# Kernel optimization log

Measured on AMD Instinct MI355X. Metric: run time of the kernel, lower is better.

Reference implementation:

```python
import jax, jax.numpy as jnp
import numpy as np

B, S, D, F, H = 32768, 3, 512, 512, 8
DH = F // H
NEG = 1e9


def setup_inputs() -> dict:
    key = jax.random.key(0)
    ks = jax.random.split(key, 13)
    mk = lambda i, shape: jax.random.normal(ks[i], shape, dtype=jnp.float32)
    return {
        "q": mk(0, (B, S, D)),
        "k": mk(1, (B, S, D)),
        "v": mk(2, (B, S, D)),
        "mask": jax.random.randint(ks[3], (B, S), 0, 2, dtype=jnp.int32),
        "Wq": mk(4, (D, F)) * 0.02, "bq": jnp.zeros((F,), jnp.float32),
        "Wk": mk(5, (D, F)) * 0.02, "bk": jnp.zeros((F,), jnp.float32),
        "Wv": mk(6, (D, F)) * 0.02, "bv": jnp.zeros((F,), jnp.float32),
        "Wo": mk(7, (F, F)) * 0.02, "bo": jnp.zeros((F,), jnp.float32),
    }


def _split_heads(x):
    # [B, S, F] -> [B, H, S, DH]
    b, s, _ = x.shape
    return x.reshape(b, s, H, DH).transpose(0, 2, 1, 3)


def reference(q, k, v, mask, Wq, bq, Wk, bk, Wv, bv, Wo, bo):
    qh = _split_heads(q @ Wq + bq)
    kh = _split_heads(k @ Wk + bk)
    vh = _split_heads(v @ Wv + bv)
    scores = jnp.einsum("bhqd,bhkd->bhqk", qh, kh) / np.sqrt(DH).astype(np.float32)
    m = mask.astype(scores.dtype) * NEG  # [B, S]
    scores = scores - m[:, None, None, :] - m[:, None, :, None]  # col + row mask
    w = jax.nn.softmax(scores, axis=-1)
    attn = jnp.einsum("bhqk,bhkd->bhqd", w, vh)  # [B, H, S, DH]
    attn = attn.transpose(0, 2, 1, 3).reshape(attn.shape[0], S, F)
    return attn @ Wo + bo
```

## Files before the change

### kernel.cpp

```cpp
#include <hip/hip_runtime.h>


typedef __bf16 bf16x8 __attribute__((ext_vector_type(8)));
typedef float f32x4 __attribute__((ext_vector_type(4)));

union U8 { bf16x8 v; unsigned short u[8]; uint4 q; };

__device__ __forceinline__ unsigned short f2bf(float f) {
  union { float f; unsigned int u; } v; v.f = f;
  unsigned int u = v.u;
  return (unsigned short)((u + 0x7FFFu + ((u >> 16) & 1u)) >> 16);
}
__device__ __forceinline__ unsigned int cvt_pk_bf16(float lo, float hi) {
  unsigned int r;
  asm volatile("v_cvt_pk_bf16_f32 %0, %1, %2" : "=v"(r) : "v"(lo), "v"(hi));
  return r;
}

__global__ void __launch_bounds__(256) wtrans(const float* __restrict__ W0,
                                              const float* __restrict__ W1,
                                              const float* __restrict__ W2,
                                              const float* __restrict__ W3,
                                              unsigned short* __restrict__ out) {
  __shared__ float tile[64][65];
  const float* W = (blockIdx.z == 0) ? W0 : (blockIdx.z == 1) ? W1
                   : (blockIdx.z == 2) ? W2 : W3;
  unsigned short* O = out + (size_t)blockIdx.z * 512 * 512;
  int t = threadIdx.x;
  int k0 = blockIdx.x * 64, n0 = blockIdx.y * 64;
#pragma unroll
  for (int i = 0; i < 4; ++i) {
    int r = (t >> 4) + i * 16;
    int c = (t & 15) * 4;
    float4 v = *(const float4*)(W + (k0 + r) * 512 + n0 + c);
    tile[r][c] = v.x; tile[r][c + 1] = v.y; tile[r][c + 2] = v.z; tile[r][c + 3] = v.w;
  }
  __syncthreads();
  int lane = t & 63, f = t >> 6;
  int lr = lane & 15, hi = lane >> 4;
#pragma unroll
  for (int i = 0; i < 2; ++i) {
    int g = f + i * 4;
    int n16l = g & 3, ksl = g >> 2;
    U8 pk;
#pragma unroll
    for (int e = 0; e < 8; ++e)
      pk.u[e] = f2bf(tile[ksl * 32 + hi * 8 + e][n16l * 16 + lr]);
    int n16 = (n0 >> 4) + n16l;
    int ksg = (k0 >> 5) + ksl;
    *(uint4*)(O + (((n16 * 16 + ksg) * 64 + lane) * 8)) = pk.q;
  }
}

#define SH_SCR  49152
#define SH_PS   65536
#define SH_MSK  71680
#define SH_BIAS 71872

__device__ __forceinline__ void stage48(const float* __restrict__ src, int row0,
                                        int t, char* smem) {
#pragma unroll 1
  for (int c = 0; c < 3; ++c) {
    float4 vals[4];
#pragma unroll
    for (int j = 0; j < 4; ++j) {
      int idx = t + (c * 4 + j) * 512;
      int row = idx >> 7, c4 = idx & 127;
      vals[j] = *(const float4*)(src + (size_t)(row0 + row) * 512 + c4 * 4);
    }
#pragma unroll
    for (int j = 0; j < 4; ++j) {
      int idx = t + (c * 4 + j) * 512;
      int row = idx >> 7, c4 = idx & 127;
      uint2 pk;
      pk.x = cvt_pk_bf16(vals[j].x, vals[j].y);
      pk.y = cvt_pk_bf16(vals[j].z, vals[j].w);
      *(uint2*)(smem + ((row * 1024 + c4 * 8) ^ ((row & 7) << 4))) = pk;
    }
  }
}

__device__ __forceinline__ void gemm_proj(const char* smem,
                                          const unsigned short* __restrict__ Bt,
                                          int w, int l, int lr, int lk8,
                                          f32x4 acc[3][4]) {
#pragma unroll 2
  for (int ks = 0; ks < 16; ++ks) {
    int kb = ks * 32 + lk8;
    bf16x8 a[3];
#pragma unroll
    for (int mt = 0; mt < 3; ++mt) {
      int row = mt * 16 + lr;
      a[mt] = *(const bf16x8*)(smem + ((row * 1024 + kb * 2) ^ ((row & 7) << 4)));
    }
#pragma unroll
    for (int np = 0; np < 2; ++np) {
      bf16x8 b[2];
#pragma unroll
      for (int j = 0; j < 2; ++j)
        b[j] = *(const bf16x8*)(Bt + (((w * 4 + np * 2 + j) * 16 + ks) * 64 + l) * 8);
#pragma unroll
      for (int j = 0; j < 2; ++j)
#pragma unroll
        for (int mt = 0; mt < 3; ++mt)
          acc[mt][np * 2 + j] =
              __builtin_amdgcn_mfma_f32_16x16x32_bf16(a[mt], b[j], acc[mt][np * 2 + j], 0, 0, 0);
    }
  }
}

__device__ __forceinline__ void tile_to_afrags(char* scr, const float* biasT, int bofs,
                                               const f32x4 acc[4], float scale,
                                               int lr, int hi, bf16x8* out) {
#pragma unroll
  for (int nt = 0; nt < 4; ++nt) {
    float bv = biasT[bofs + nt * 16];
#pragma unroll
    for (int r = 0; r < 4; ++r) {
      int row = 4 * hi + r;
      int col = nt * 16 + lr;
      int addr = (row * 128 + col * 2) ^ ((row & 7) << 4);
      *(unsigned short*)(scr + addr) = f2bf((acc[nt][r] + bv) * scale);
    }
  }
  asm volatile("s_waitcnt lgkmcnt(0)" ::: "memory");
#pragma unroll
  for (int kb = 0; kb < 2; ++kb) {
    int addr = (lr * 128 + (kb * 32 + hi * 8) * 2) ^ ((lr & 7) << 4);
    out[kb] = *(const bf16x8*)(scr + addr);
  }
  asm volatile("s_waitcnt lgkmcnt(0)" ::: "memory");
}

__global__ void __launch_bounds__(512, 4) fused_attn(
    const float* __restrict__ q, const float* __restrict__ kin, const float* __restrict__ vin,
    const int* __restrict__ mask, const unsigned short* __restrict__ wt,
    const float* __restrict__ bq, const float* __restrict__ bk,
    const float* __restrict__ bv, const float* __restrict__ bo,
    float* __restrict__ out) {
  __shared__ alignas(16) char smem[80064];
  const int t = threadIdx.x;
  const int w = t >> 6;
  const int l = t & 63;
  const int lr = l & 15;
  const int hi = l >> 4;
  const int lk8 = hi * 8;
  const int row0 = blockIdx.x * 48;
  const int batch0 = blockIdx.x * 16;
  char* scr = smem + SH_SCR + w * 2048;
  float* pscr = (float*)(smem + SH_PS + w * 768);
  int* maskb = (int*)(smem + SH_MSK);
  float* biasT = (float*)(smem + SH_BIAS);
  const int bidx = w * 64 + lr;

  if (t < 48) maskb[t] = mask[batch0 * 3 + t];
  biasT[0 * 512 + t] = bq[t];
  biasT[1 * 512 + t] = bk[t];
  biasT[2 * 512 + t] = bv[t];
  biasT[3 * 512 + t] = bo[t];

  const unsigned short* Wtq = wt;
  const unsigned short* Wtk = wt + 512 * 512;
  const unsigned short* Wtv = wt + 2 * 512 * 512;
  const unsigned short* Wto = wt + 3 * 512 * 512;

  stage48(q, row0, t, smem);
  __syncthreads();
  bf16x8 qa[3][2];
  {
    f32x4 aq[3][4] = {};
    gemm_proj(smem, Wtq, w, l, lr, lk8, aq);
#pragma unroll
    for (int mt = 0; mt < 3; ++mt)
      tile_to_afrags(scr, biasT, 0 * 512 + bidx, aq[mt], 0.125f, lr, hi, qa[mt]);
  }
  __syncthreads();

  stage48(kin, row0, t, smem);
  __syncthreads();
  {
    f32x4 ack[3][4] = {};
    gemm_proj(smem, Wtk, w, l, lr, lk8, ack);

    bf16x8 kf[3][2];
#pragma unroll
    for (int km = 0; km < 3; ++km)
      tile_to_afrags(scr, biasT, 1 * 512 + bidx, ack[km], 1.0f, lr, hi, kf[km]);

#pragma unroll
    for (int km = 0; km < 3; ++km) {
      f32x4 s[3] = {};
#pragma unroll
      for (int qm = 0; qm < 3; ++qm) {
        s[qm] = __builtin_amdgcn_mfma_f32_16x16x32_bf16(qa[qm][0], kf[km][0], s[qm], 0, 0, 0);
        s[qm] = __builtin_amdgcn_mfma_f32_16x16x32_bf16(qa[qm][1], kf[km][1], s[qm], 0, 0, 0);
      }
#pragma unroll
      for (int qm = 0; qm < 3; ++qm)
#pragma unroll
        for (int r = 0; r < 4; ++r) {
          int qrow = qm * 16 + hi * 4 + r;
          int krow = km * 16 + lr;
          int qb = qrow / 3, kb2 = krow / 3;
          if (qb == kb2) pscr[qrow * 4 + (krow - kb2 * 3)] = s[qm][r];
        }
    }
    asm volatile("s_waitcnt lgkmcnt(0)" ::: "memory");
#pragma unroll
    for (int mt = 0; mt < 3; ++mt) {
      int row = mt * 16 + lr;
      int b = row / 3;
      int qi = row - b * 3;
      float s0 = pscr[row * 4 + 0], s1 = pscr[row * 4 + 1], s2 = pscr[row * 4 + 2];
      float m0 = (float)maskb[b * 3 + 0] * 1e9f;
      float m1 = (float)maskb[b * 3 + 1] * 1e9f;
      float m2 = (float)maskb[b * 3 + 2] * 1e9f;
      float mq = (qi == 0) ? m0 : (qi == 1) ? m1 : m2;
      float t0 = (s0 - m0) - mq;
      float t1 = (s1 - m1) - mq;
      float t2 = (s2 - m2) - mq;
      float mx = fmaxf(fmaxf(t0, t1), t2);
      float e0 = __expf(t0 - mx), e1 = __expf(t1 - mx), e2 = __expf(t2 - mx);
      float inv = 1.0f / (e0 + e1 + e2);
      asm volatile("s_waitcnt lgkmcnt(0)" ::: "memory");
      pscr[row * 4 + 0] = e0 * inv;
      pscr[row * 4 + 1] = e1 * inv;
      pscr[row * 4 + 2] = e2 * inv;
    }
  }
  __syncthreads();

  stage48(vin, row0, t, smem);
  __syncthreads();
  f32x4 acv[3][4] = {};
  gemm_proj(smem, Wtv, w, l, lr, lk8, acv);

  bf16x8 vb2[2][4];
  {
    U8 zz;
#pragma unroll
    for (int e = 0; e < 8; ++e) zz.u[e] = 0;
#pragma unroll
    for (int nt = 0; nt < 4; ++nt) vb2[1][nt] = zz.v;
  }
#pragma unroll
  for (int mt = 0; mt < 3; ++mt) {
#pragma unroll
    for (int nt = 0; nt < 4; ++nt) {
      float bvl = biasT[2 * 512 + bidx + nt * 16];
      int d = nt * 16 + lr;
      uint2 pk;
      pk.x = cvt_pk_bf16(acv[mt][nt][0] + bvl, acv[mt][nt][1] + bvl);
      pk.y = cvt_pk_bf16(acv[mt][nt][2] + bvl, acv[mt][nt][3] + bvl);
      *(uint2*)(scr + ((d * 32 + hi * 8) ^ ((d & 1) << 4))) = pk;
    }
    asm volatile("s_waitcnt lgkmcnt(0)" ::: "memory");
#pragma unroll
    for (int nt = 0; nt < 4; ++nt) {
      int d = nt * 16 + lr;
      bf16x8 tmp = *(const bf16x8*)(scr + ((d * 32 + (hi & 1) * 16) ^ ((d & 1) << 4)));
      if (mt == 0)      { if (hi < 2)  vb2[0][nt] = tmp; }
      else if (mt == 1) { if (hi >= 2) vb2[0][nt] = tmp; }
      else              { if (hi < 2)  vb2[1][nt] = tmp; }
    }
    asm volatile("s_waitcnt lgkmcnt(0)" ::: "memory");
  }
  bf16x8 pa[3][2];
#pragma unroll
  for (int mt = 0; mt < 3; ++mt) {
    int row = mt * 16 + lr;
    int b3 = (row / 3) * 3;
    float pr0 = pscr[row * 4 + 0];
    float pr1 = pscr[row * 4 + 1];
    float pr2 = pscr[row * 4 + 2];
#pragma unroll
    for (int kb = 0; kb < 2; ++kb) {
      U8 f;
#pragma unroll
      for (int e = 0; e < 8; ++e) {
        int k = kb * 32 + lk8 + e;
        int j = k - b3;
        float pv_ = (j == 0) ? pr0 : (j == 1) ? pr1 : (j == 2) ? pr2 : 0.f;
        f.u[e] = f2bf(pv_);
      }
      pa[mt][kb] = f.v;
    }
  }
  f32x4 pv[3][4] = {};
#pragma unroll
  for (int kb = 0; kb < 2; ++kb)
#pragma unroll
    for (int nt = 0; nt < 4; ++nt)
#pragma unroll
      for (int mt = 0; mt < 3; ++mt)
        pv[mt][nt] = __builtin_amdgcn_mfma_f32_16x16x32_bf16(pa[mt][kb], vb2[kb][nt], pv[mt][nt], 0, 0, 0);

  __syncthreads();
#pragma unroll
  for (int mt = 0; mt < 3; ++mt)
#pragma unroll
    for (int nt = 0; nt < 4; ++nt)
#pragma unroll
      for (int r = 0; r < 4; ++r) {
        int row = mt * 16 + hi * 4 + r;
        int col = w * 64 + nt * 16 + lr;
        *(unsigned short*)(smem + ((row * 1024 + col * 2) ^ ((row & 7) << 4))) =
            f2bf(pv[mt][nt][r]);
      }
  __syncthreads();

  f32x4 ao[3][4] = {};
  gemm_proj(smem, Wto, w, l, lr, lk8, ao);
#pragma unroll
  for (int mt = 0; mt < 3; ++mt)
#pragma unroll
    for (int nt = 0; nt < 4; ++nt) {
      float bvo = biasT[3 * 512 + bidx + nt * 16];
#pragma unroll
      for (int r = 0; r < 4; ++r) {
        int grow = row0 + mt * 16 + hi * 4 + r;
        int col = w * 64 + nt * 16 + lr;
        out[(size_t)grow * 512 + col] = ao[mt][nt][r] + bvo;
      }
    }
}

extern "C" void kernel_launch(void* const* d_in, const int* in_sizes, int n_in,
                              void* d_out, int out_size, void* d_ws, size_t ws_size,
                              hipStream_t stream) {
  const float* q = (const float*)d_in[0];
  const float* k = (const float*)d_in[1];
  const float* v = (const float*)d_in[2];
  const int* mask = (const int*)d_in[3];
  const float* Wq = (const float*)d_in[4];
  const float* bq = (const float*)d_in[5];
  const float* Wk = (const float*)d_in[6];
  const float* bk = (const float*)d_in[7];
  const float* Wv = (const float*)d_in[8];
  const float* bv = (const float*)d_in[9];
  const float* Wo = (const float*)d_in[10];
  const float* bo = (const float*)d_in[11];
  float* out = (float*)d_out;
  unsigned short* wt = (unsigned short*)d_ws;

  wtrans<<<dim3(8, 8, 4), 256, 0, stream>>>(Wq, Wk, Wv, Wo, wt);
  fused_attn<<<2048, 512, 0, stream>>>(q, k, v, mask, wt, bq, bk, bv, bo, out);
}
```

Measured before the change: 421.0 us.

## Double-buffer input staging in K-halves to overlap global loads with MFMA

Splits each 48x512 input staging into two 256-column halves held in two LDS buffers, and issues the global loads for the next half (or the next tensor) into registers before running the GEMM on the current half. The goal is to hide global-memory latency for the q/k/v reads behind the projection MFMAs instead of stalling on full staging between phases. The block syncs are replaced by a custom barrier using sched_barrier and an lgkmcnt wait. The 24 prefetched float4 values per thread add register pressure, which could affect the 4-blocks-per-CU occupancy target.

Result: slower. 591.2 us (+40.4%).

```diff
diff --git a/kernel.cpp b/kernel.cpp
--- a/kernel.cpp
+++ b/kernel.cpp
@@ -15,6 +15,13 @@
   unsigned int r;
   asm volatile("v_cvt_pk_bf16_f32 %0, %1, %2" : "=v"(r) : "v"(lo), "v"(hi));
   return r;
+}
+
+__device__ __forceinline__ void block_sync() {
+  __builtin_amdgcn_sched_barrier(0);
+  asm volatile("s_waitcnt lgkmcnt(0)" ::: "memory");
+  __builtin_amdgcn_s_barrier();
+  __builtin_amdgcn_sched_barrier(0);
 }
 
 __global__ void __launch_bounds__(256) wtrans(const float* __restrict__ W0,
@@ -52,53 +59,54 @@
   }
 }
 
+#define SH_A    0
+#define SH_B    24576
 #define SH_SCR  49152
 #define SH_PS   65536
 #define SH_MSK  71680
 #define SH_BIAS 71872
 
-__device__ __forceinline__ void stage48(const float* __restrict__ src, int row0,
-                                        int t, char* smem) {
-#pragma unroll 1
-  for (int c = 0; c < 3; ++c) {
-    float4 vals[4];
-#pragma unroll
-    for (int j = 0; j < 4; ++j) {
-      int idx = t + (c * 4 + j) * 512;
-      int row = idx >> 7, c4 = idx & 127;
-      vals[j] = *(const float4*)(src + (size_t)(row0 + row) * 512 + c4 * 4);
-    }
-#pragma unroll
-    for (int j = 0; j < 4; ++j) {
-      int idx = t + (c * 4 + j) * 512;
-      int row = idx >> 7, c4 = idx & 127;
-      uint2 pk;
-      pk.x = cvt_pk_bf16(vals[j].x, vals[j].y);
-      pk.y = cvt_pk_bf16(vals[j].z, vals[j].w);
-      *(uint2*)(smem + ((row * 1024 + c4 * 8) ^ ((row & 7) << 4))) = pk;
-    }
-  }
-}
-
-__device__ __forceinline__ void gemm_proj(const char* smem,
+__device__ __forceinline__ void stage_issue(const float* __restrict__ src, int row0,
+                                            int half, int t, float4* pre) {
+#pragma unroll
+  for (int i = 0; i < 6; ++i) {
+    int idx = t + i * 512;
+    int row = idx >> 6, c4 = idx & 63;
+    pre[i] = *(const float4*)(src + (size_t)(row0 + row) * 512 + half * 256 + c4 * 4);
+  }
+  __builtin_amdgcn_sched_barrier(0);
+}
+__device__ __forceinline__ void stage_write(char* buf, int t, const float4* pre) {
+#pragma unroll
+  for (int i = 0; i < 6; ++i) {
+    int idx = t + i * 512;
+    int row = idx >> 6, c4 = idx & 63;
+    uint2 pk;
+    pk.x = cvt_pk_bf16(pre[i].x, pre[i].y);
+    pk.y = cvt_pk_bf16(pre[i].z, pre[i].w);
+    *(uint2*)(buf + ((row * 512 + c4 * 8) ^ ((row & 7) << 4))) = pk;
+  }
+}
+
+__device__ __forceinline__ void gemm_half(const char* buf,
                                           const unsigned short* __restrict__ Bt,
-                                          int w, int l, int lr, int lk8,
+                                          int gksb, int w, int l, int lr, int lk8,
                                           f32x4 acc[3][4]) {
 #pragma unroll 2
-  for (int ks = 0; ks < 16; ++ks) {
-    int kb = ks * 32 + lk8;
+  for (int ks = 0; ks < 8; ++ks) {
+    int kl = ks * 32 + lk8;
     bf16x8 a[3];
 #pragma unroll
     for (int mt = 0; mt < 3; ++mt) {
       int row = mt * 16 + lr;
-      a[mt] = *(const bf16x8*)(smem + ((row * 1024 + kb * 2) ^ ((row & 7) << 4)));
+      a[mt] = *(const bf16x8*)(buf + ((row * 512 + kl * 2) ^ ((row & 7) << 4)));
     }
 #pragma unroll
     for (int np = 0; np < 2; ++np) {
       bf16x8 b[2];
 #pragma unroll
       for (int j = 0; j < 2; ++j)
-        b[j] = *(const bf16x8*)(Bt + (((w * 4 + np * 2 + j) * 16 + ks) * 64 + l) * 8);
+        b[j] = *(const bf16x8*)(Bt + (((w * 4 + np * 2 + j) * 16 + (gksb + ks)) * 64 + l) * 8);
 #pragma unroll
       for (int j = 0; j < 2; ++j)
 #pragma unroll
@@ -147,6 +155,8 @@
   const int lk8 = hi * 8;
   const int row0 = blockIdx.x * 48;
   const int batch0 = blockIdx.x * 16;
+  char* bufA = smem + SH_A;
+  char* bufB = smem + SH_B;
   char* scr = smem + SH_SCR + w * 2048;
   float* pscr = (float*)(smem + SH_PS + w * 768);
   int* maskb = (int*)(smem + SH_MSK);
@@ -164,29 +174,44 @@
   const unsigned short* Wtv = wt + 2 * 512 * 512;
   const unsigned short* Wto = wt + 3 * 512 * 512;
 
-  stage48(q, row0, t, smem);
-  __syncthreads();
+  float4 pre[6];
+
+  stage_issue(q, row0, 0, t, pre);
+  stage_write(bufA, t, pre);
+  block_sync();
+  stage_issue(q, row0, 1, t, pre);
+
   bf16x8 qa[3][2];
   {
     f32x4 aq[3][4] = {};
-    gemm_proj(smem, Wtq, w, l, lr, lk8, aq);
+    gemm_half(bufA, Wtq, 0, w, l, lr, lk8, aq);
+    stage_write(bufB, t, pre);
+    block_sync();
+    stage_issue(kin, row0, 0, t, pre);
+    gemm_half(bufB, Wtq, 8, w, l, lr, lk8, aq);
+    stage_write(bufA, t, pre);
+    block_sync();
+    stage_issue(kin, row0, 1, t, pre);
 #pragma unroll
     for (int mt = 0; mt < 3; ++mt)
       tile_to_afrags(scr, biasT, 0 * 512 + bidx, aq[mt], 0.125f, lr, hi, qa[mt]);
   }
-  __syncthreads();
-
-  stage48(kin, row0, t, smem);
-  __syncthreads();
+
   {
     f32x4 ack[3][4] = {};
-    gemm_proj(smem, Wtk, w, l, lr, lk8, ack);
+    gemm_half(bufA, Wtk, 0, w, l, lr, lk8, ack);
+    stage_write(bufB, t, pre);
+    block_sync();
+    stage_issue(vin, row0, 0, t, pre);
+    gemm_half(bufB, Wtk, 8, w, l, lr, lk8, ack);
+    stage_write(bufA, t, pre);
+    block_sync();
+    stage_issue(vin, row0, 1, t, pre);
 
     bf16x8 kf[3][2];
 #pragma unroll
     for (int km = 0; km < 3; ++km)
       tile_to_afrags(scr, biasT, 1 * 512 + bidx, ack[km], 1.0f, lr, hi, kf[km]);
-
 #pragma unroll
     for (int km = 0; km < 3; ++km) {
       f32x4 s[3] = {};
@@ -228,12 +253,12 @@
       pscr[row * 4 + 2] = e2 * inv;
     }
   }
-  __syncthreads();
-
-  stage48(vin, row0, t, smem);
-  __syncthreads();
+
   f32x4 acv[3][4] = {};
-  gemm_proj(smem, Wtv, w, l, lr, lk8, acv);
+  gemm_half(bufA, Wtv, 0, w, l, lr, lk8, acv);
+  stage_write(bufB, t, pre);
+  block_sync();
+  gemm_half(bufB, Wtv, 8, w, l, lr, lk8, acv);
 
   bf16x8 vb2[2][4];
   {
@@ -295,22 +320,27 @@
       for (int mt = 0; mt < 3; ++mt)
         pv[mt][nt] = __builtin_amdgcn_mfma_f32_16x16x32_bf16(pa[mt][kb], vb2[kb][nt], pv[mt][nt], 0, 0, 0);
 
-  __syncthreads();
-#pragma unroll
-  for (int mt = 0; mt < 3; ++mt)
-#pragma unroll
-    for (int nt = 0; nt < 4; ++nt)
-#pragma unroll
-      for (int r = 0; r < 4; ++r) {
-        int row = mt * 16 + hi * 4 + r;
-        int col = w * 64 + nt * 16 + lr;
-        *(unsigned short*)(smem + ((row * 1024 + col * 2) ^ ((row & 7) << 4))) =
-            f2bf(pv[mt][nt][r]);
-      }
-  __syncthreads();
+  block_sync();
+  {
+    char* abuf = (w < 4) ? bufA : bufB;
+    int cw = (w & 3) * 64;
+#pragma unroll
+    for (int mt = 0; mt < 3; ++mt)
+#pragma unroll
+      for (int nt = 0; nt < 4; ++nt)
+#pragma unroll
+        for (int r = 0; r < 4; ++r) {
+          int row = mt * 16 + hi * 4 + r;
+          int colh = cw + nt * 16 + lr;
+          *(unsigned short*)(abuf + ((row * 512 + colh * 2) ^ ((row & 7) << 4))) =
+              f2bf(pv[mt][nt][r]);
+        }
+  }
+  block_sync();
 
   f32x4 ao[3][4] = {};
-  gemm_proj(smem, Wto, w, l, lr, lk8, ao);
+  gemm_half(bufA, Wto, 0, w, l, lr, lk8, ao);
+  gemm_half(bufB, Wto, 8, w, l, lr, lk8, ao);
 #pragma unroll
   for (int mt = 0; mt < 3; ++mt)
 #pragma unroll
```

## Load Q/K/V projection A-fragments directly from global instead of staging in LDS

Applied to the files above, without the earlier changes.

The Q, K and V projection GEMMs now read each wave's A-operand fragments straight from global fp32 memory and convert them to bf16 in registers. This drops the cooperative LDS staging pass and several block-wide barriers. The cost is that each of the 8 waves redundantly fetches the same 48x512 input rows, relying on L1/L2 to absorb the repeats, and global-load latency now sits inside the MFMA loop. The B-fragment loads are also regrouped so all four are issued before the MFMAs.

Measured after the change: 786.3 us. +86.8%, slower.

```diff
diff --git a/kernel.cpp b/kernel.cpp
--- a/kernel.cpp
+++ b/kernel.cpp
@@ -4,7 +4,7 @@
 typedef __bf16 bf16x8 __attribute__((ext_vector_type(8)));
 typedef float f32x4 __attribute__((ext_vector_type(4)));
 
-union U8 { bf16x8 v; unsigned short u[8]; uint4 q; };
+union U8 { bf16x8 v; unsigned short u[8]; unsigned int w[4]; uint4 q; };
 
 __device__ __forceinline__ unsigned short f2bf(float f) {
   union { float f; unsigned int u; } v; v.f = f;
@@ -52,38 +52,47 @@
   }
 }
 
+#define SH_ATT  0
 #define SH_SCR  49152
 #define SH_PS   65536
 #define SH_MSK  71680
 #define SH_BIAS 71872
 
-__device__ __forceinline__ void stage48(const float* __restrict__ src, int row0,
-                                        int t, char* smem) {
-#pragma unroll 1
-  for (int c = 0; c < 3; ++c) {
-    float4 vals[4];
-#pragma unroll
-    for (int j = 0; j < 4; ++j) {
-      int idx = t + (c * 4 + j) * 512;
-      int row = idx >> 7, c4 = idx & 127;
-      vals[j] = *(const float4*)(src + (size_t)(row0 + row) * 512 + c4 * 4);
-    }
-#pragma unroll
-    for (int j = 0; j < 4; ++j) {
-      int idx = t + (c * 4 + j) * 512;
-      int row = idx >> 7, c4 = idx & 127;
-      uint2 pk;
-      pk.x = cvt_pk_bf16(vals[j].x, vals[j].y);
-      pk.y = cvt_pk_bf16(vals[j].z, vals[j].w);
-      *(uint2*)(smem + ((row * 1024 + c4 * 8) ^ ((row & 7) << 4))) = pk;
-    }
-  }
-}
-
-__device__ __forceinline__ void gemm_proj(const char* smem,
-                                          const unsigned short* __restrict__ Bt,
-                                          int w, int l, int lr, int lk8,
-                                          f32x4 acc[3][4]) {
+__device__ __forceinline__ void gemm_dir(const float* __restrict__ Aw,
+                                         const unsigned short* __restrict__ Bt,
+                                         int w, int l, f32x4 acc[3][4]) {
+#pragma unroll 2
+  for (int ks = 0; ks < 16; ++ks) {
+    bf16x8 a[3];
+#pragma unroll
+    for (int mt = 0; mt < 3; ++mt) {
+      const float* p = Aw + mt * (16 * 512) + ks * 32;
+      float4 lo = *(const float4*)(p);
+      float4 hp = *(const float4*)(p + 4);
+      U8 f;
+      f.w[0] = cvt_pk_bf16(lo.x, lo.y);
+      f.w[1] = cvt_pk_bf16(lo.z, lo.w);
+      f.w[2] = cvt_pk_bf16(hp.x, hp.y);
+      f.w[3] = cvt_pk_bf16(hp.z, hp.w);
+      a[mt] = f.v;
+    }
+    bf16x8 b[4];
+#pragma unroll
+    for (int nt = 0; nt < 4; ++nt)
+      b[nt] = *(const bf16x8*)(Bt + (((w * 4 + nt) * 16 + ks) * 64 + l) * 8);
+#pragma unroll
+    for (int nt = 0; nt < 4; ++nt)
+#pragma unroll
+      for (int mt = 0; mt < 3; ++mt)
+        acc[mt][nt] =
+            __builtin_amdgcn_mfma_f32_16x16x32_bf16(a[mt], b[nt], acc[mt][nt], 0, 0, 0);
+  }
+}
+
+__device__ __forceinline__ void gemm_lds(const char* buf,
+                                         const unsigned short* __restrict__ Bt,
+                                         int w, int l, int lr, int lk8,
+                                         f32x4 acc[3][4]) {
 #pragma unroll 2
   for (int ks = 0; ks < 16; ++ks) {
     int kb = ks * 32 + lk8;
@@ -91,21 +100,18 @@
 #pragma unroll
     for (int mt = 0; mt < 3; ++mt) {
       int row = mt * 16 + lr;
-      a[mt] = *(const bf16x8*)(smem + ((row * 1024 + kb * 2) ^ ((row & 7) << 4)));
-    }
-#pragma unroll
-    for (int np = 0; np < 2; ++np) {
-      bf16x8 b[2];
-#pragma unroll
-      for (int j = 0; j < 2; ++j)
-        b[j] = *(const bf16x8*)(Bt + (((w * 4 + np * 2 + j) * 16 + ks) * 64 + l) * 8);
-#pragma unroll
-      for (int j = 0; j < 2; ++j)
-#pragma unroll
-        for (int mt = 0; mt < 3; ++mt)
-          acc[mt][np * 2 + j] =
-              __builtin_amdgcn_mfma_f32_16x16x32_bf16(a[mt], b[j], acc[mt][np * 2 + j], 0, 0, 0);
-    }
+      a[mt] = *(const bf16x8*)(buf + ((row * 1024 + kb * 2) ^ ((row & 7) << 4)));
+    }
+    bf16x8 b[4];
+#pragma unroll
+    for (int nt = 0; nt < 4; ++nt)
+      b[nt] = *(const bf16x8*)(Bt + (((w * 4 + nt) * 16 + ks) * 64 + l) * 8);
+#pragma unroll
+    for (int nt = 0; nt < 4; ++nt)
+#pragma unroll
+      for (int mt = 0; mt < 3; ++mt)
+        acc[mt][nt] =
+            __builtin_amdgcn_mfma_f32_16x16x32_bf16(a[mt], b[nt], acc[mt][nt], 0, 0, 0);
   }
 }
 
@@ -147,6 +153,7 @@
   const int lk8 = hi * 8;
   const int row0 = blockIdx.x * 48;
   const int batch0 = blockIdx.x * 16;
+  char* attnb = smem + SH_ATT;
   char* scr = smem + SH_SCR + w * 2048;
   float* pscr = (float*)(smem + SH_PS + w * 768);
   int* maskb = (int*)(smem + SH_MSK);
@@ -164,23 +171,21 @@
   const unsigned short* Wtv = wt + 2 * 512 * 512;
   const unsigned short* Wto = wt + 3 * 512 * 512;
 
-  stage48(q, row0, t, smem);
-  __syncthreads();
+  const size_t abase = (size_t)(row0 + lr) * 512 + hi * 8;
+
   bf16x8 qa[3][2];
   {
     f32x4 aq[3][4] = {};
-    gemm_proj(smem, Wtq, w, l, lr, lk8, aq);
+    gemm_dir(q + abase, Wtq, w, l, aq);
+    __syncthreads();
 #pragma unroll
     for (int mt = 0; mt < 3; ++mt)
       tile_to_afrags(scr, biasT, 0 * 512 + bidx, aq[mt], 0.125f, lr, hi, qa[mt]);
   }
-  __syncthreads();
-
-  stage48(kin, row0, t, smem);
-  __syncthreads();
+
   {
     f32x4 ack[3][4] = {};
-    gemm_proj(smem, Wtk, w, l, lr, lk8, ack);
+    gemm_dir(kin + abase, Wtk, w, l, ack);
 
     bf16x8 kf[3][2];
 #pragma unroll
@@ -228,12 +233,9 @@
       pscr[row * 4 + 2] = e2 * inv;
     }
   }
-  __syncthreads();
-
-  stage48(vin, row0, t, smem);
-  __syncthreads();
+
   f32x4 acv[3][4] = {};
-  gemm_proj(smem, Wtv, w, l, lr, lk8, acv);
+  gemm_dir(vin + abase, Wtv, w, l, acv);
 
   bf16x8 vb2[2][4];
   {
@@ -295,7 +297,6 @@
       for (int mt = 0; mt < 3; ++mt)
         pv[mt][nt] = __builtin_amdgcn_mfma_f32_16x16x32_bf16(pa[mt][kb], vb2[kb][nt], pv[mt][nt], 0, 0, 0);
 
-  __syncthreads();
 #pragma unroll
   for (int mt = 0; mt < 3; ++mt)
 #pragma unroll
@@ -304,13 +305,13 @@
       for (int r = 0; r < 4; ++r) {
         int row = mt * 16 + hi * 4 + r;
         int col = w * 64 + nt * 16 + lr;
-        *(unsigned short*)(smem + ((row * 1024 + col * 2) ^ ((row & 7) << 4))) =
+        *(unsigned short*)(attnb + ((row * 1024 + col * 2) ^ ((row & 7) << 4))) =
             f2bf(pv[mt][nt][r]);
       }
   __syncthreads();
 
   f32x4 ao[3][4] = {};
-  gemm_proj(smem, Wto, w, l, lr, lk8, ao);
+  gemm_lds(attnb, Wto, w, l, lr, lk8, ao);
 #pragma unroll
   for (int mt = 0; mt < 3; ++mt)
 #pragma unroll
```
